# Optimization experiments

Measured on AMD Instinct MI355X. Metric: run time of the kernel, lower is better.

## Reference

```python
import jax, jax.numpy as jnp
import numpy as np

N = 200000      # nodes
E = 1600000     # edges
B = 1000        # graphs
SD = 64         # state_dim
AD = 32         # action_dim
H = 128         # HIDDEN_LAYER
EPS = 1e-5


def setup_inputs() -> dict:
    key = jax.random.key(0)
    ks = jax.random.split(key, 16)
    x = jax.random.normal(ks[0], (N, SD), dtype=jnp.float32)
    action = jax.random.normal(ks[1], (N, AD), dtype=jnp.float32)
    edge_index = jax.random.randint(ks[2], (2, E), 0, N, dtype=jnp.int64)
    batch_size = jnp.sort(jax.random.randint(ks[3], (N,), 0, B, dtype=jnp.int64))
    # parameters (Linear weights stored [in, out]; torch init std=0.1 for fc layers)
    W_gcn = jax.random.normal(ks[4], (SD, H), dtype=jnp.float32) / np.sqrt(SD)
    b_gcn = jnp.zeros((H,), jnp.float32)
    g0 = jnp.ones((H,), jnp.float32); be0 = jnp.zeros((H,), jnp.float32)
    W1 = jax.random.normal(ks[5], (H, H), dtype=jnp.float32) * 0.1
    b1 = jnp.zeros((H,), jnp.float32)
    g1 = jnp.ones((H,), jnp.float32); be1 = jnp.zeros((H,), jnp.float32)
    W2 = jax.random.normal(ks[6], (AD, H), dtype=jnp.float32) * 0.1
    b2 = jnp.zeros((H,), jnp.float32)
    g2 = jnp.ones((H,), jnp.float32); be2 = jnp.zeros((H,), jnp.float32)
    W3 = jax.random.normal(ks[7], (2 * H, 1), dtype=jnp.float32) * 0.1
    b3 = jnp.zeros((1,), jnp.float32)
    return dict(x=x, action=action, W_gcn=W_gcn, b_gcn=b_gcn, g0=g0, be0=be0,
                W1=W1, b1=b1, g1=g1, be1=be1, W2=W2, b2=b2, g2=g2, be2=be2,
                W3=W3, b3=b3, edge_index=edge_index, batch_size=batch_size)


def _bn(h, gamma, beta):
    # BatchNorm1d, training-mode batch statistics over the node axis
    mu = jnp.mean(h, axis=0)
    var = jnp.var(h, axis=0)
    return (h - mu) * jax.lax.rsqrt(var + EPS) * gamma + beta


def _gcn(x, edge_index, W, b):
    # GCN conv with self-loops and symmetric normalization:
    # out_i = sum_{j in N(i) u {i}} (d_i d_j)^{-1/2} (x_j W) + b
    loops = jnp.arange(N, dtype=edge_index.dtype)
    src = jnp.concatenate([edge_index[0], loops])
    dst = jnp.concatenate([edge_index[1], loops])
    deg = jax.ops.segment_sum(jnp.ones_like(dst, dtype=x.dtype), dst, num_segments=N)
    dinv = jax.lax.rsqrt(deg)                       # deg >= 1 due to self-loops
    norm = dinv[src] * dinv[dst]                    # [E+N]
    xw = x @ W                                      # [N, H]
    msg = xw[src] * norm[:, None]                   # [E+N, H]
    return jax.ops.segment_sum(msg, dst, num_segments=N) + b


def reference(x, action, W_gcn, b_gcn, g0, be0, W1, b1, g1, be1,
              W2, b2, g2, be2, W3, b3, edge_index, batch_size):
    h0 = jax.nn.relu(_gcn(x, edge_index, W_gcn, b_gcn))
    h0n = _bn(h0, g0, be0)
    h1 = jax.nn.relu(h0n @ W1 + b1)
    h1n = _bn(h1, g1, be1)
    h2 = jax.nn.relu(action @ W2 + b2)
    h2n = _bn(h2, g2, be2)
    feat = jnp.concatenate([h1n, h2n], axis=1)      # [N, 2H]
    sums = jax.ops.segment_sum(feat, batch_size, num_segments=B)
    cnts = jax.ops.segment_sum(jnp.ones((N,), feat.dtype), batch_size, num_segments=B)
    pooled = sums / jnp.maximum(cnts, 1.0)[:, None]  # [B, 2H]
    return pooled @ W3 + b3                          # [B, 1]
```

## Files before the change

kernel.cpp:

```cpp
#include <hip/hip_runtime.h>

typedef unsigned short u16;
typedef unsigned int   u32;
typedef __bf16 bf16x8 __attribute__((ext_vector_type(8)));
typedef float  f32x4  __attribute__((ext_vector_type(4)));

#define EPS 1e-5f
#define BSHIFT 9

__device__ __forceinline__ float b2f(u16 u){ union{u32 i; float f;} v; v.i=((u32)u)<<16; return v.f; }
__device__ __forceinline__ u16 f2b(float f){
  u32 x = __float_as_uint(f);
  u32 r = x + 0x7fffu + ((x>>16)&1u);
  return (u16)(r>>16);
}

template<int K, bool RELU, bool HASBIAS, bool AF32, bool POOL>
__device__ __forceinline__ void gemm_body(const void* __restrict__ Av,
                                          const u16* __restrict__ BhiT,
                                          const u16* __restrict__ BloT,
                                          const float* __restrict__ bias,
                                          u16* __restrict__ C,
                                          float* __restrict__ stats,
                                          const int* __restrict__ batch,
                                          float* __restrict__ P, int M,
                                          int bid, int halfg)
{
  constexpr int KM = K / 8;
  constexpr int KR = K / 32;
  constexpr int GCAP = 8;
  extern __shared__ char smem[];
  u16* lds    = (u16*)smem;
  float* sred = (float*)(smem + (size_t)2 * 64 * K * 2);
  float* qred = sred + 64;
  u16*  sbatch = (u16*)(qred + 64);
  float* Pacc  = (float*)(sbatch + 1024);
  const int tid = threadIdx.x;
  const int ch = (bid >= halfg) ? 1 : 0;
  const int t0 = bid - ch * halfg;
  for (int i = tid; i < 64 * KM; i += 256) {
    const int n = i / KM, kb = i % KM;
    const int kb2 = kb ^ (n & (KM - 1));
    const int gsrc = ((ch * 64 + n) * KM + kb) * 8;
    *(uint4*)(&lds[(n * KM + kb2) * 8])          = *(const uint4*)(BhiT + gsrc);
    *(uint4*)(&lds[64 * K + (n * KM + kb2) * 8]) = *(const uint4*)(BloT + gsrc);
  }
  if (tid < 64) { sred[tid] = 0.f; qred[tid] = 0.f; }
  const int nmt = (M + 127) >> 7;
  int mt_begin, mt_end, mt_step, rlo = 0;
  if (POOL) {
    const int qt = nmt / halfg, rm = nmt % halfg;
    mt_begin = (t0 < rm) ? t0 * (qt + 1) : rm * (qt + 1) + (t0 - rm) * qt;
    mt_end   = mt_begin + ((t0 < rm) ? qt + 1 : qt);
    mt_step  = 1;
    rlo = mt_begin << 7;
    const int rcnt = min(mt_end << 7, M) - rlo;
    for (int i = tid; i < rcnt; i += 256) sbatch[i] = (u16)batch[rlo + i];
    for (int i = tid; i < GCAP * 64; i += 256) Pacc[i] = 0.f;
  } else {
    mt_begin = t0; mt_end = nmt; mt_step = halfg;
  }
  __syncthreads();
  const int g_lo = POOL ? (int)sbatch[0] : 0;
  const int wid = tid >> 6, lane = tid & 63, q = lane >> 4, r16 = lane & 15;
  float ls[4], lq[4];
#pragma unroll
  for (int nb = 0; nb < 4; nb++) { ls[nb] = 0.f; lq[nb] = 0.f; }
  float bv[4];
#pragma unroll
  for (int nb = 0; nb < 4; nb++) bv[nb] = HASBIAS ? bias[ch * 64 + nb * 16 + r16] : 0.f;

  for (int mt = mt_begin; mt < mt_end; mt += mt_step) {
    const int row0 = mt << 7;
    const bool ok1 = (row0 + 64) < M;

    bf16x8 av[2][KR];
    if (AF32) {
      const float* Af = (const float*)Av + (size_t)(row0 + (wid << 4) + r16) * K + q * 8;
#pragma unroll
      for (int kk = 0; kk < KR; kk++) {
        f32x4 x0 = *(const f32x4*)(Af + kk * 32);
        f32x4 x1 = *(const f32x4*)(Af + kk * 32 + 4);
#pragma unroll
        for (int j = 0; j < 4; j++) { av[0][kk][j] = (__bf16)x0[j]; av[0][kk][4 + j] = (__bf16)x1[j]; }
      }
      if (ok1) {
        const float* Ag = Af + (size_t)64 * K;
#pragma unroll
        for (int kk = 0; kk < KR; kk++) {
          f32x4 x0 = *(const f32x4*)(Ag + kk * 32);
          f32x4 x1 = *(const f32x4*)(Ag + kk * 32 + 4);
#pragma unroll
          for (int j = 0; j < 4; j++) { av[1][kk][j] = (__bf16)x0[j]; av[1][kk][4 + j] = (__bf16)x1[j]; }
        }
      }
    } else {
      const u16* Ab = (const u16*)Av + (size_t)(row0 + (wid << 4) + r16) * K + q * 8;
#pragma unroll
      for (int kk = 0; kk < KR; kk++) av[0][kk] = *(const bf16x8*)(Ab + kk * 32);
      if (ok1) {
#pragma unroll
        for (int kk = 0; kk < KR; kk++) av[1][kk] = *(const bf16x8*)(Ab + (size_t)64 * K + kk * 32);
      }
    }

    f32x4 acc[2][4];
#pragma unroll
    for (int rt = 0; rt < 2; rt++)
#pragma unroll
      for (int nb = 0; nb < 4; nb++) acc[rt][nb] = (f32x4){0.f, 0.f, 0.f, 0.f};
#pragma unroll
    for (int kk = 0; kk < KR; kk++) {
#pragma unroll
      for (int nb = 0; nb < 4; nb++) {
        const int n = nb * 16 + r16;
        const int kb2 = (kk * 4 + q) ^ (n & (KM - 1));
        const bf16x8 bh = *(const bf16x8*)(&lds[(n * KM + kb2) * 8]);
        const bf16x8 bl = *(const bf16x8*)(&lds[64 * K + (n * KM + kb2) * 8]);
        acc[0][nb] = __builtin_amdgcn_mfma_f32_16x16x32_bf16(av[0][kk], bh, acc[0][nb], 0, 0, 0);
        acc[0][nb] = __builtin_amdgcn_mfma_f32_16x16x32_bf16(av[0][kk], bl, acc[0][nb], 0, 0, 0);
        if (ok1) {
          acc[1][nb] = __builtin_amdgcn_mfma_f32_16x16x32_bf16(av[1][kk], bh, acc[1][nb], 0, 0, 0);
          acc[1][nb] = __builtin_amdgcn_mfma_f32_16x16x32_bf16(av[1][kk], bl, acc[1][nb], 0, 0, 0);
        }
      }
    }

#pragma unroll
    for (int rt = 0; rt < 2; rt++) {
      if (rt && !ok1) continue;
      const int rbase = row0 + rt * 64 + (wid << 4) + (q << 2);
#pragma unroll
      for (int nb = 0; nb < 4; nb++) {
        const int col = ch * 64 + nb * 16 + r16;
#pragma unroll
        for (int r = 0; r < 4; r++) {
          float v = acc[rt][nb][r] + bv[nb];
          if (RELU) v = fmaxf(v, 0.f);
          ls[nb] += v; lq[nb] += v * v;
          if (!POOL) C[(size_t)(rbase + r) * 128 + col] = f2b(v);
          else acc[rt][nb][r] = v;
        }
      }
      if (POOL) {
        int bg[4];
#pragma unroll
        for (int r = 0; r < 4; r++) bg[r] = (int)sbatch[rbase - rlo + r];
        const int g0 = __shfl(bg[0], 0, 64);
        const int g1 = __shfl(bg[3], 48, 64);
        for (int g = g0; g <= g1; ++g) {
#pragma unroll
          for (int nb = 0; nb < 4; nb++) {
            float sv = 0.f;
#pragma unroll
            for (int r = 0; r < 4; r++) sv += (bg[r] == g) ? acc[rt][nb][r] : 0.f;
            sv += __shfl_xor(sv, 16, 64);
            sv += __shfl_xor(sv, 32, 64);
            if (q == 0) {
              const int gi = g - g_lo;
              if ((unsigned)gi < GCAP) atomicAdd(&Pacc[gi * 64 + nb * 16 + r16], sv);
              else atomicAdd(&P[g * 128 + ch * 64 + nb * 16 + r16], sv);
            }
          }
        }
      }
    }
  }
#pragma unroll
  for (int nb = 0; nb < 4; nb++) {
    atomicAdd(&sred[nb * 16 + r16], ls[nb]);
    atomicAdd(&qred[nb * 16 + r16], lq[nb]);
  }
  __syncthreads();
  if (tid < 64) {
    atomicAdd(&stats[ch * 64 + tid], sred[tid]);
    atomicAdd(&stats[128 + ch * 64 + tid], qred[tid]);
  }
  if (POOL) {
    for (int i = tid; i < GCAP * 64; i += 256) {
      const float v = Pacc[i];
      if (v != 0.f) atomicAdd(&P[(g_lo + (i >> 6)) * 128 + ch * 64 + (i & 63)], v);
    }
  }
}

template<int K, bool RELU, bool HASBIAS, bool AF32, bool POOL>
__global__ __launch_bounds__(256) void k_gemm(const void* __restrict__ Av,
                                              const u16* __restrict__ BhiT,
                                              const u16* __restrict__ BloT,
                                              const float* __restrict__ bias,
                                              u16* __restrict__ C,
                                              float* __restrict__ stats,
                                              const int* __restrict__ batch,
                                              float* __restrict__ P, int M)
{
  gemm_body<K, RELU, HASBIAS, AF32, POOL>(Av, BhiT, BloT, bias, C, stats, batch, P, M,
                                          blockIdx.x, gridDim.x >> 1);
}

__global__ __launch_bounds__(256) void k_gemm2(const void* __restrict__ A1,
                                               const u16* __restrict__ B1hi,
                                               const u16* __restrict__ B1lo,
                                               const float* __restrict__ bias1,
                                               float* __restrict__ stats1,
                                               float* __restrict__ P1,
                                               const void* __restrict__ A2,
                                               const u16* __restrict__ B2hi,
                                               const u16* __restrict__ B2lo,
                                               const float* __restrict__ bias2,
                                               float* __restrict__ stats2,
                                               float* __restrict__ P2,
                                               const int* __restrict__ batch,
                                               int M, int g1blk, int g2blk)
{
  if ((int)blockIdx.x < g1blk)
    gemm_body<128, true, true, false, true>(A1, B1hi, B1lo, bias1, nullptr, stats1,
                                            batch, P1, M, blockIdx.x, g1blk >> 1);
  else
    gemm_body<32, true, true, true, true>(A2, B2hi, B2lo, bias2, nullptr, stats2,
                                          batch, P2, M, blockIdx.x - g1blk, g2blk >> 1);
}

__global__ void k_prep0(const float* __restrict__ Wg, const float* __restrict__ W2,
                        u16* __restrict__ WghiT, u16* __restrict__ WgloT,
                        u16* __restrict__ W2hiT, u16* __restrict__ W2loT,
                        const int* __restrict__ batch, int* __restrict__ gofs,
                        int* __restrict__ zbase, int zwords, int NZ, int N, int B)
{
  const int bid = blockIdx.x, t = threadIdx.x;
  if (bid < NZ) {
    const int i = bid * 2048 + t * 8;
    if (i < zwords) {
      *(int4*)(zbase + i)     = make_int4(0, 0, 0, 0);
      *(int4*)(zbase + i + 4) = make_int4(0, 0, 0, 0);
    }
  } else if (bid < NZ + 48) {
    const int i = (bid - NZ) * 256 + t;
    if (i < 64 * 128) {
      int k = i >> 7, n = i & 127;
      float w = Wg[i]; u16 h = f2b(w);
      WghiT[n * 64 + k] = h; WgloT[n * 64 + k] = f2b(w - b2f(h));
    } else if (i < 64 * 128 + 32 * 128) {
      int j = i - 64 * 128;
      int k = j >> 7, n = j & 127;
      float w = W2[j]; u16 h = f2b(w);
      W2hiT[n * 32 + k] = h; W2loT[n * 32 + k] = f2b(w - b2f(h));
    }
  } else {
    const int i = (bid - NZ - 48) * 256 + t;
    if (i == 0) { for (int g = 0; g <= batch[0]; g++) gofs[g] = 0; }
    if (i == N - 1) { for (int g = batch[N - 1] + 1; g <= B; g++) gofs[g] = N; }
    if (i < N - 1) {
      const int b0 = batch[i], b1 = batch[i + 1];
      for (int g = b0 + 1; g <= b1; g++) gofs[g] = i + 1;
    }
  }
}

__global__ __launch_bounds__(256) void k_bincnt(const int* __restrict__ dst, int* __restrict__ btot,
                                                int E, int NB)
{
  extern __shared__ int hist[];
  const int tid = threadIdx.x;
  for (int i = tid; i < NB; i += 256) hist[i] = 0;
  __syncthreads();
  const int chunk = (E + gridDim.x - 1) / gridDim.x;
  const int start = blockIdx.x * chunk;
  const int end = min(start + chunk, E);
  for (int e = start + tid; e < end; e += 256) atomicAdd(&hist[((u32)dst[e]) >> BSHIFT], 1);
  __syncthreads();
  for (int i = tid; i < NB; i += 256) if (hist[i]) atomicAdd(&btot[i], hist[i]);
}

__global__ __launch_bounds__(256) void k_bin(const int* __restrict__ src, const int* __restrict__ dst,
                                             const int* __restrict__ btot, int* __restrict__ bcur,
                                             int* __restrict__ bbase_out,
                                             uint2* __restrict__ pairs, int E, int NB)
{
  extern __shared__ int lds[];
  int* sb    = lds;
  int* hist  = lds + NB;
  int* wbase = lds + 2 * NB;
  int* sscan = lds + 3 * NB;
  const int tid = threadIdx.x;
  const int per = (NB + 255) / 256;
  int loc[4]; int sum = 0;
  for (int j = 0; j < per; j++) { int idx = tid * per + j; int v = (idx < NB) ? btot[idx] : 0; loc[j] = sum; sum += v; }
  sscan[tid] = sum; __syncthreads();
  for (int o = 1; o < 256; o <<= 1) {
    int x = (tid >= o) ? sscan[tid - o] : 0;
    __syncthreads();
    sscan[tid] += x;
    __syncthreads();
  }
  const int ex = sscan[tid] - sum;
  for (int j = 0; j < per; j++) {
    int idx = tid * per + j;
    if (idx < NB) {
      sb[idx] = ex + loc[j];
      if (blockIdx.x == 0) bbase_out[idx] = ex + loc[j];
    }
  }
  if (blockIdx.x == 0 && tid == 255) bbase_out[NB] = sscan[255];
  for (int i = tid; i < NB; i += 256) hist[i] = 0;
  __syncthreads();
  const int chunk = (E + gridDim.x - 1) / gridDim.x;
  const int start = blockIdx.x * chunk;
  const int end = min(start + chunk, E);
  for (int e = start + tid; e < end; e += 256) atomicAdd(&hist[((u32)dst[e]) >> BSHIFT], 1);
  __syncthreads();
  for (int i = tid; i < NB; i += 256) {
    int c = hist[i];
    wbase[i] = c ? sb[i] + atomicAdd(&bcur[i], c) : 0;
    hist[i] = 0;
  }
  __syncthreads();
  for (int e = start + tid; e < end; e += 256) {
    const int d = dst[e];
    const int b = ((u32)d) >> BSHIFT;
    const int o = atomicAdd(&hist[b], 1);
    pairs[wbase[b] + o] = make_uint2((u32)d, (u32)src[e]);
  }
}

__global__ __launch_bounds__(512) void k_bucket(const uint2* __restrict__ pairs,
                                                const int* __restrict__ bbase,
                                                const float* __restrict__ x,
                                                int* __restrict__ offsets, float* __restrict__ dinv,
                                                int* __restrict__ elist, u16* __restrict__ y,
                                                int N, int NB, int Etot)
{
  __shared__ int hist[512];
  __shared__ int scn[512];
  __shared__ int lcur[512];
  __shared__ float sdinv[512];
  const int b = blockIdx.x, t = threadIdx.x;
  const int nbase = b << BSHIFT;
  const int nn = min(1 << BSHIFT, N - nbase);
  hist[t] = 0;
  __syncthreads();
  const int p0 = bbase[b], p1 = bbase[b + 1];
  for (int p = p0 + t; p < p1; p += 512) atomicAdd(&hist[pairs[p].x - nbase], 1);
  __syncthreads();
  const int h = hist[t];
  scn[t] = h; __syncthreads();
  for (int o = 1; o < 512; o <<= 1) {
    int xx = (t >= o) ? scn[t - o] : 0;
    __syncthreads();
    scn[t] += xx;
    __syncthreads();
  }
  const int ex = scn[t] - h;
  if (t < nn) {
    const int i = nbase + t;
    const int off = p0 + ex + i;
    const float d = rsqrtf((float)(h + 1));
    offsets[i] = off; elist[off] = i; lcur[t] = off + 1;
    dinv[i] = d; sdinv[t] = d;
  }
  if (b == NB - 1 && t == 0) offsets[N] = Etot;
  __syncthreads();
  for (int p = p0 + t; p < p1; p += 512) {
    const uint2 pr = pairs[p];
    const int pos = atomicAdd(&lcur[pr.x - nbase], 1);
    elist[pos] = (int)pr.y;
  }
  const size_t ebase = (size_t)nbase * 64;
  const int total = nn * 64;
  for (int i = t * 8; i < total; i += 512 * 8) {
    const float d = sdinv[i >> 6];
    f32x4 a = *(const f32x4*)(x + ebase + i);
    f32x4 c = *(const f32x4*)(x + ebase + i + 4);
    u16 o[8];
#pragma unroll
    for (int j = 0; j < 4; j++) { o[j] = f2b(a[j] * d); o[4 + j] = f2b(c[j] * d); }
    *(uint4*)(y + ebase + i) = *(uint4*)o;
  }
}

__global__ __launch_bounds__(256) void k_agg(const u16* __restrict__ y, const int* __restrict__ offsets,
                                             const int* __restrict__ elist, const float* __restrict__ dinv,
                                             u16* __restrict__ aggx, int n)
{
  const int lane = threadIdx.x & 63;
  const int half = lane >> 5, l32 = lane & 31;
  const int g4 = l32 >> 3, sub = lane & 7;
  const int wid  = (blockIdx.x * 256 + threadIdx.x) >> 6;
  const int nw   = gridDim.x * 4;
  const int npair = (n + 1) >> 1;
  for (int pr = wid; pr < npair; pr += nw) {
    const int node = pr * 2 + half;
    const int s0 = offsets[node], s1 = offsets[node + 1];
    const int mydeg = s1 - s0;
    const int degA = __shfl(mydeg, 0, 64);
    const int degB = __shfl(mydeg, 32, 64);
    const int degmax = max(degA, degB);
    float a[8];
#pragma unroll
    for (int t = 0; t < 8; t++) a[t] = 0.f;
    for (int base = 0; base < degmax; base += 32) {
      const int m = mydeg - base;
      const int ev = (base + l32 < mydeg) ? elist[s0 + base + l32] : 0;
      const int iters = (min(32, degmax - base) + 3) >> 2;
      for (int it = 0; it < iters; it++) {
        const int j = it * 4 + g4;
        const int idx = __shfl(ev, half * 32 + j, 64);
        if (j < m) {
          const uint4 v = *(const uint4*)(y + (size_t)idx * 64 + sub * 8);
          const u32 w[4] = {v.x, v.y, v.z, v.w};
#pragma unroll
          for (int t = 0; t < 4; t++) {
            a[2 * t]     += b2f((u16)w[t]);
            a[2 * t + 1] += b2f((u16)(w[t] >> 16));
          }
        }
      }
    }
#pragma unroll
    for (int t = 0; t < 8; t++) {
      a[t] += __shfl_xor(a[t], 8, 64);
      a[t] += __shfl_xor(a[t], 16, 64);
    }
    if (g4 == 0) {
      const float di = dinv[node];
      u16 o[8];
#pragma unroll
      for (int t = 0; t < 8; t++) o[t] = f2b(a[t] * di);
      *(uint4*)(aggx + (size_t)node * 64 + sub * 8) = *(uint4*)o;
    }
  }
}

__global__ void k_prep1(const float* __restrict__ stats0, const float* __restrict__ W1,
                        const float* __restrict__ b1, const float* __restrict__ g0,
                        const float* __restrict__ be0, u16* __restrict__ W1hiT,
                        u16* __restrict__ W1loT, float* __restrict__ b1p, float n)
{
  __shared__ float A[8], Csh[8];
  const int t = threadIdx.x;
  if (t < 8) {
    const int k = blockIdx.x * 8 + t;
    const float mu = stats0[k] / n;
    const float var = fmaxf(stats0[128 + k] / n - mu * mu, 0.f);
    const float a = g0[k] * rsqrtf(var + EPS);
    A[t] = a; Csh[t] = be0[k] - mu * a;
  }
  __syncthreads();
  float acc = (blockIdx.x == 0) ? b1[t] : 0.f;
#pragma unroll
  for (int kk = 0; kk < 8; kk++) {
    const int k = blockIdx.x * 8 + kk;
    const float w0 = W1[k * 128 + t];
    acc += Csh[kk] * w0;
    const float w = A[kk] * w0;
    const u16 h = f2b(w);
    W1hiT[t * 128 + k] = h;
    W1loT[t * 128 + k] = f2b(w - b2f(h));
  }
  atomicAdd(&b1p[t], acc);
}

__global__ void k_out3(const float* __restrict__ P1, const float* __restrict__ P2,
                       const int* __restrict__ gofs,
                       const float* __restrict__ stats1, const float* __restrict__ stats2,
                       const float* __restrict__ g1, const float* __restrict__ be1,
                       const float* __restrict__ g2, const float* __restrict__ be2,
                       const float* __restrict__ W3, const float* __restrict__ b3,
                       float* __restrict__ out, int B, float n)
{
  __shared__ float w1s[128], w2s[128], red[256], cS[2];
  const int t = threadIdx.x;
  float c, wv;
  if (t < 128) {
    const float mu = stats1[t] / n;
    const float var = fmaxf(stats1[128 + t] / n - mu * mu, 0.f);
    const float a = g1[t] * rsqrtf(var + EPS);
    c = be1[t] - mu * a;
    wv = W3[t];
    w1s[t] = a * wv;
  } else {
    const int f = t - 128;
    const float mu = stats2[f] / n;
    const float var = fmaxf(stats2[128 + f] / n - mu * mu, 0.f);
    const float a = g2[f] * rsqrtf(var + EPS);
    c = be2[f] - mu * a;
    wv = W3[t];
    w2s[f] = a * wv;
  }
  red[t] = c * wv; __syncthreads();
  for (int o = 128; o; o >>= 1) { if (t < o) red[t] += red[t + o]; __syncthreads(); }
  if (t == 0) { cS[0] = red[0] + b3[0]; cS[1] = b3[0]; }
  __syncthreads();
  const int lane = t & 63;
  const int g = (blockIdx.x * 256 + t) >> 6;
  if (g >= B) return;
  const int cnt = gofs[g + 1] - gofs[g];
  const int k = 2 * lane;
  float d = P1[g * 128 + k] * w1s[k] + P1[g * 128 + k + 1] * w1s[k + 1]
          + P2[g * 128 + k] * w2s[k] + P2[g * 128 + k + 1] * w2s[k + 1];
#pragma unroll
  for (int o = 1; o < 64; o <<= 1) d += __shfl_xor(d, o, 64);
  if (lane == 0) out[g] = (cnt > 0) ? d / (float)cnt + cS[0] : cS[1];
}

extern "C" void kernel_launch(void* const* d_in, const int* in_sizes, int n_in,
                              void* d_out, int out_size, void* d_ws, size_t ws_size,
                              hipStream_t stream)
{
  const float* x    = (const float*)d_in[0];
  const float* act  = (const float*)d_in[1];
  const float* Wg   = (const float*)d_in[2];
  const float* bg   = (const float*)d_in[3];
  const float* g0   = (const float*)d_in[4];
  const float* be0  = (const float*)d_in[5];
  const float* W1   = (const float*)d_in[6];
  const float* b1   = (const float*)d_in[7];
  const float* g1   = (const float*)d_in[8];
  const float* be1  = (const float*)d_in[9];
  const float* W2   = (const float*)d_in[10];
  const float* b2   = (const float*)d_in[11];
  const float* g2   = (const float*)d_in[12];
  const float* be2  = (const float*)d_in[13];
  const float* W3   = (const float*)d_in[14];
  const float* b3   = (const float*)d_in[15];
  const int* eidx   = (const int*)d_in[16];
  const int* batch  = (const int*)d_in[17];

  const int N = in_sizes[17];
  const int E = in_sizes[16] / 2;
  const int B = out_size;
  const int* src = eidx;
  const int* dst = eidx + E;
  const int NB = (N + (1 << BSHIFT) - 1) >> BSHIFT;

  char* ws = (char*)d_ws;
  size_t off = 0;
  auto alloc = [&](size_t bytes) -> char* {
    off = (off + 255) & ~(size_t)255;
    char* p = ws + off; off += bytes; return p;
  };

  u16* bufA = (u16*)alloc((size_t)N * 128 * 2);
  u16* xb   = (u16*)alloc((size_t)N * 64 * 2);
  u16* aggx = (u16*)alloc((size_t)N * 64 * 2);

  int zwords = 768 + 128 + 2 * NB + 2 * 128 * B;
  zwords = (zwords + 7) & ~7;
  char* zbase   = alloc((size_t)zwords * 4);
  float* stats0 = (float*)zbase;
  float* stats1 = stats0 + 256;
  float* stats2 = stats1 + 256;
  float* b1p    = stats2 + 256;
  int*   btot   = (int*)(b1p + 128);
  int*   bcur   = btot + NB;
  float* P1     = (float*)(bcur + NB);
  float* P2     = P1 + 128 * B;

  int*   offsets = (int*)alloc((size_t)(N + 1) * 4);
  float* dinv    = (float*)alloc((size_t)N * 4);
  int*   elist   = (int*)alloc((size_t)(E + N) * 4);
  uint2* pairs   = (uint2*)alloc((size_t)E * 8);
  int*   bbase   = (int*)alloc((size_t)(NB + 1) * 4);
  int*   gofs    = (int*)alloc((size_t)(B + 1) * 4);
  u16*   WghiT   = (u16*)alloc(128 * 64 * 2);
  u16*   WgloT   = (u16*)alloc(128 * 64 * 2);
  u16*   W1hiT   = (u16*)alloc(128 * 128 * 2);
  u16*   W1loT   = (u16*)alloc(128 * 128 * 2);
  u16*   W2hiT   = (u16*)alloc(128 * 32 * 2);
  u16*   W2loT   = (u16*)alloc(128 * 32 * 2);

  u16* h0 = bufA;

  const int smem64  = 2 * 64 * 64 * 2 + 512;
  const int smem128 = 2 * 64 * 128 * 2 + 512 + 2048 + 2048;
  const int smembin = (3 * NB + 256) * 4;

  const int NZ = (zwords + 2047) / 2048;
  const int nbounds = (N + 255) / 256;
  k_prep0<<<NZ + 48 + nbounds, 256, 0, stream>>>(Wg, W2, WghiT, WgloT, W2hiT, W2loT,
                                                 batch, gofs, (int*)zbase, zwords, NZ, N, B);
  k_bincnt<<<512, 256, NB * 4, stream>>>(dst, btot, E, NB);
  k_bin<<<512, 256, smembin, stream>>>(src, dst, btot, bcur, bbase, pairs, E, NB);
  k_bucket<<<NB, 512, 0, stream>>>(pairs, bbase, x, offsets, dinv, elist, xb, N, NB, E + N);
  k_agg<<<2048, 256, 0, stream>>>(xb, offsets, elist, dinv, aggx, N);
  k_gemm<64, true, true, false, false><<<768, 256, smem64, stream>>>(aggx, WghiT, WgloT, bg,
                                                                     h0, stats0, nullptr, nullptr, N);
  k_prep1<<<16, 128, 0, stream>>>(stats0, W1, b1, g0, be0, W1hiT, W1loT, b1p, (float)N);
  k_gemm2<<<768 + 512, 256, smem128, stream>>>(h0, W1hiT, W1loT, b1p, stats1, P1,
                                               act, W2hiT, W2loT, b2, stats2, P2,
                                               batch, N, 768, 512);
  k_out3<<<(B * 64 + 255) / 256, 256, 0, stream>>>(P1, P2, gofs, stats1, stats2,
                                                   g1, be1, g2, be2, W3, b3,
                                                   (float*)d_out, B, (float)N);
}
```

Before: 366.4 us.

## Fuse GCN neighbor aggregation with the first GEMM through an LDS tile

Replaces the separate aggregation kernel and the first GEMM with one kernel. Each 512-thread block gathers 128 node rows into a shared-memory tile, then runs MFMA against the hi/lo split weights held in LDS and emits h0 with ReLU plus BN statistics. This removes the aggx round trip through global memory and one launch. In exchange each block now has a fixed node range instead of a grid-stride loop, which can cause load imbalance across blocks. Large LDS use (about 52KB static) may also reduce occupancy for the gather-heavy phase.

New measurement: 449.9 us. 1.23x slower.

```diff
diff --git a/kernel.cpp b/kernel.cpp
--- a/kernel.cpp
+++ b/kernel.cpp
@@ -184,20 +184,6 @@
   }
 }
 
-template<int K, bool RELU, bool HASBIAS, bool AF32, bool POOL>
-__global__ __launch_bounds__(256) void k_gemm(const void* __restrict__ Av,
-                                              const u16* __restrict__ BhiT,
-                                              const u16* __restrict__ BloT,
-                                              const float* __restrict__ bias,
-                                              u16* __restrict__ C,
-                                              float* __restrict__ stats,
-                                              const int* __restrict__ batch,
-                                              float* __restrict__ P, int M)
-{
-  gemm_body<K, RELU, HASBIAS, AF32, POOL>(Av, BhiT, BloT, bias, C, stats, batch, P, M,
-                                          blockIdx.x, gridDim.x >> 1);
-}
-
 __global__ __launch_bounds__(256) void k_gemm2(const void* __restrict__ A1,
                                                const u16* __restrict__ B1hi,
                                                const u16* __restrict__ B1lo,
@@ -219,6 +205,127 @@
   else
     gemm_body<32, true, true, true, true>(A2, B2hi, B2lo, bias2, nullptr, stats2,
                                           batch, P2, M, blockIdx.x - g1blk, g2blk >> 1);
+}
+
+__global__ __launch_bounds__(512) void k_aggemm(const u16* __restrict__ y,
+                                                const int* __restrict__ offsets,
+                                                const int* __restrict__ elist,
+                                                const float* __restrict__ dinv,
+                                                const u16* __restrict__ WhiT,
+                                                const u16* __restrict__ WloT,
+                                                const float* __restrict__ bias,
+                                                u16* __restrict__ C,
+                                                float* __restrict__ stats, int M)
+{
+  __shared__ u16 wlds[2 * 128 * 64];
+  __shared__ u16 atile[128 * 72];
+  __shared__ float sred[128], qred[128];
+  const int tid = threadIdx.x;
+  for (int i = tid; i < 128 * 8; i += 512) {
+    const int n = i >> 3, kb = i & 7;
+    const int kb2 = kb ^ (n & 7);
+    *(uint4*)(&wlds[(n * 8 + kb2) * 8])            = *(const uint4*)(WhiT + i * 8);
+    *(uint4*)(&wlds[128 * 64 + (n * 8 + kb2) * 8]) = *(const uint4*)(WloT + i * 8);
+  }
+  if (tid < 128) { sred[tid] = 0.f; qred[tid] = 0.f; }
+
+  const int rowb = blockIdx.x << 7;
+  const bool ok1 = (rowb + 64) < M;
+  const int wid = tid >> 6, lane = tid & 63;
+  const int half = lane >> 5, l32 = lane & 31;
+  const int g4 = l32 >> 3, sub = lane & 7;
+
+  if (wid < 4 || ok1) {
+    for (int pr = 0; pr < 8; pr++) {
+      const int node = rowb + (wid << 4) + pr * 2 + half;
+      const int s0 = offsets[node], s1 = offsets[node + 1];
+      const int mydeg = s1 - s0;
+      const int degA = __shfl(mydeg, 0, 64);
+      const int degB = __shfl(mydeg, 32, 64);
+      const int degmax = max(degA, degB);
+      float a[8];
+#pragma unroll
+      for (int t = 0; t < 8; t++) a[t] = 0.f;
+      for (int base = 0; base < degmax; base += 32) {
+        const int m = mydeg - base;
+        const int ev = (base + l32 < mydeg) ? elist[s0 + base + l32] : 0;
+        const int iters = (min(32, degmax - base) + 3) >> 2;
+        for (int it = 0; it < iters; it++) {
+          const int j = it * 4 + g4;
+          const int idx = __shfl(ev, half * 32 + j, 64);
+          if (j < m) {
+            const uint4 v = *(const uint4*)(y + (size_t)idx * 64 + sub * 8);
+            const u32 w[4] = {v.x, v.y, v.z, v.w};
+#pragma unroll
+            for (int t = 0; t < 4; t++) {
+              a[2 * t]     += b2f((u16)w[t]);
+              a[2 * t + 1] += b2f((u16)(w[t] >> 16));
+            }
+          }
+        }
+      }
+#pragma unroll
+      for (int t = 0; t < 8; t++) {
+        a[t] += __shfl_xor(a[t], 8, 64);
+        a[t] += __shfl_xor(a[t], 16, 64);
+      }
+      if (g4 == 0) {
+        const float di = dinv[node];
+        u16 o[8];
+#pragma unroll
+        for (int t = 0; t < 8; t++) o[t] = f2b(a[t] * di);
+        const int lrow = (wid << 4) + pr * 2 + half;
+        *(uint4*)(&atile[lrow * 72 + sub * 8]) = *(uint4*)o;
+      }
+    }
+  }
+  __syncthreads();
+
+  const int q = lane >> 4, r16 = lane & 15;
+  float ls[8], lq[8];
+#pragma unroll
+  for (int nb = 0; nb < 8; nb++) { ls[nb] = 0.f; lq[nb] = 0.f; }
+  if (wid < 4 || ok1) {
+    bf16x8 av[2];
+#pragma unroll
+    for (int kk = 0; kk < 2; kk++)
+      av[kk] = *(const bf16x8*)(&atile[((wid << 4) + r16) * 72 + kk * 32 + q * 8]);
+    f32x4 acc[8];
+#pragma unroll
+    for (int nb = 0; nb < 8; nb++) acc[nb] = (f32x4){0.f, 0.f, 0.f, 0.f};
+#pragma unroll
+    for (int kk = 0; kk < 2; kk++) {
+#pragma unroll
+      for (int nb = 0; nb < 8; nb++) {
+        const int n = nb * 16 + r16;
+        const int kb2 = (kk * 4 + q) ^ (n & 7);
+        const bf16x8 bh = *(const bf16x8*)(&wlds[(n * 8 + kb2) * 8]);
+        const bf16x8 bl = *(const bf16x8*)(&wlds[128 * 64 + (n * 8 + kb2) * 8]);
+        acc[nb] = __builtin_amdgcn_mfma_f32_16x16x32_bf16(av[kk], bh, acc[nb], 0, 0, 0);
+        acc[nb] = __builtin_amdgcn_mfma_f32_16x16x32_bf16(av[kk], bl, acc[nb], 0, 0, 0);
+      }
+    }
+    const int rbase = rowb + (wid << 4) + (q << 2);
+#pragma unroll
+    for (int nb = 0; nb < 8; nb++) {
+      const int col = nb * 16 + r16;
+      const float bv = bias[col];
+#pragma unroll
+      for (int r = 0; r < 4; r++) {
+        float v = acc[nb][r] + bv;
+        v = fmaxf(v, 0.f);
+        ls[nb] += v; lq[nb] += v * v;
+        C[(size_t)(rbase + r) * 128 + col] = f2b(v);
+      }
+      atomicAdd(&sred[col], ls[nb]);
+      atomicAdd(&qred[col], lq[nb]);
+    }
+  }
+  __syncthreads();
+  if (tid < 128) {
+    atomicAdd(&stats[tid], sred[tid]);
+    atomicAdd(&stats[128 + tid], qred[tid]);
+  }
 }
 
 __global__ void k_prep0(const float* __restrict__ Wg, const float* __restrict__ W2,
@@ -375,59 +482,6 @@
 #pragma unroll
     for (int j = 0; j < 4; j++) { o[j] = f2b(a[j] * d); o[4 + j] = f2b(c[j] * d); }
     *(uint4*)(y + ebase + i) = *(uint4*)o;
-  }
-}
-
-__global__ __launch_bounds__(256) void k_agg(const u16* __restrict__ y, const int* __restrict__ offsets,
-                                             const int* __restrict__ elist, const float* __restrict__ dinv,
-                                             u16* __restrict__ aggx, int n)
-{
-  const int lane = threadIdx.x & 63;
-  const int half = lane >> 5, l32 = lane & 31;
-  const int g4 = l32 >> 3, sub = lane & 7;
-  const int wid  = (blockIdx.x * 256 + threadIdx.x) >> 6;
-  const int nw   = gridDim.x * 4;
-  const int npair = (n + 1) >> 1;
-  for (int pr = wid; pr < npair; pr += nw) {
-    const int node = pr * 2 + half;
-    const int s0 = offsets[node], s1 = offsets[node + 1];
-    const int mydeg = s1 - s0;
-    const int degA = __shfl(mydeg, 0, 64);
-    const int degB = __shfl(mydeg, 32, 64);
-    const int degmax = max(degA, degB);
-    float a[8];
-#pragma unroll
-    for (int t = 0; t < 8; t++) a[t] = 0.f;
-    for (int base = 0; base < degmax; base += 32) {
-      const int m = mydeg - base;
-      const int ev = (base + l32 < mydeg) ? elist[s0 + base + l32] : 0;
-      const int iters = (min(32, degmax - base) + 3) >> 2;
-      for (int it = 0; it < iters; it++) {
-        const int j = it * 4 + g4;
-        const int idx = __shfl(ev, half * 32 + j, 64);
-        if (j < m) {
-          const uint4 v = *(const uint4*)(y + (size_t)idx * 64 + sub * 8);
-          const u32 w[4] = {v.x, v.y, v.z, v.w};
-#pragma unroll
-          for (int t = 0; t < 4; t++) {
-            a[2 * t]     += b2f((u16)w[t]);
-            a[2 * t + 1] += b2f((u16)(w[t] >> 16));
-          }
-        }
-      }
-    }
-#pragma unroll
-    for (int t = 0; t < 8; t++) {
-      a[t] += __shfl_xor(a[t], 8, 64);
-      a[t] += __shfl_xor(a[t], 16, 64);
-    }
-    if (g4 == 0) {
-      const float di = dinv[node];
-      u16 o[8];
-#pragma unroll
-      for (int t = 0; t < 8; t++) o[t] = f2b(a[t] * di);
-      *(uint4*)(aggx + (size_t)node * 64 + sub * 8) = *(uint4*)o;
-    }
   }
 }
 
@@ -542,7 +596,6 @@
 
   u16* bufA = (u16*)alloc((size_t)N * 128 * 2);
   u16* xb   = (u16*)alloc((size_t)N * 64 * 2);
-  u16* aggx = (u16*)alloc((size_t)N * 64 * 2);
 
   int zwords = 768 + 128 + 2 * NB + 2 * 128 * B;
   zwords = (zwords + 7) & ~7;
@@ -571,7 +624,6 @@
 
   u16* h0 = bufA;
 
-  const int smem64  = 2 * 64 * 64 * 2 + 512;
   const int smem128 = 2 * 64 * 128 * 2 + 512 + 2048 + 2048;
   const int smembin = (3 * NB + 256) * 4;
 
@@ -582,9 +634,8 @@
   k_bincnt<<<512, 256, NB * 4, stream>>>(dst, btot, E, NB);
   k_bin<<<512, 256, smembin, stream>>>(src, dst, btot, bcur, bbase, pairs, E, NB);
   k_bucket<<<NB, 512, 0, stream>>>(pairs, bbase, x, offsets, dinv, elist, xb, N, NB, E + N);
-  k_agg<<<2048, 256, 0, stream>>>(xb, offsets, elist, dinv, aggx, N);
-  k_gemm<64, true, true, false, false><<<768, 256, smem64, stream>>>(aggx, WghiT, WgloT, bg,
-                                                                     h0, stats0, nullptr, nullptr, N);
+  k_aggemm<<<(N + 127) / 128, 512, 0, stream>>>(xb, offsets, elist, dinv,
+                                                WghiT, WgloT, bg, h0, stats0, N);
   k_prep1<<<16, 128, 0, stream>>>(stats0, W1, b1, g0, be0, W1hiT, W1loT, b1p, (float)N);
   k_gemm2<<<768 + 512, 256, smem128, stream>>>(h0, W1hiT, W1loT, b1p, stats1, P1,
                                                act, W2hiT, W2loT, b2, stats2, P2,
```
